# Performance work log

Hardware: AMD Instinct MI355X
Metric: run time of the kernel (lower is better)

The kernel has to match this reference:

```python
import jax, jax.numpy as jnp
import numpy as np

TOP_K = 2
INIT_STD = 0.02
B, T, D, E, I = 2, 2048, 1024, 8, 512


def setup_inputs() -> dict:
    key = jax.random.key(0)
    k0, k1, k2, k3, k4 = jax.random.split(key, 5)
    return {
        "x": jax.random.normal(k0, (B, T, D), dtype=jnp.float32),
        "router_w": (jax.random.normal(k1, (E, D), dtype=jnp.float32) * INIT_STD),
        "w_gate": (jax.random.normal(k2, (E, I, D), dtype=jnp.float32) * INIT_STD),
        "w_up": (jax.random.normal(k3, (E, I, D), dtype=jnp.float32) * INIT_STD),
        "w_down": (jax.random.normal(k4, (E, D, I), dtype=jnp.float32) * INIT_STD),
    }


def _moe_forward(x, router_w, w_gate, w_up, w_down):
    # x: [B, T, D]; router_w: [E, D]; w_gate/w_up: [E, I, D]; w_down: [E, D, I]
    b, t, d = x.shape
    e = router_w.shape[0]
    gate_logits = jnp.einsum('btd,ed->bte', x, router_w)          # [B, T, E]
    top_w, sel = jax.lax.top_k(gate_logits, TOP_K)                # [B, T, K]
    probs = jax.nn.softmax(top_w, axis=-1)                        # softmax over selected experts only

    n = b * t
    xf = x.reshape(n, d)                                          # [N, D]
    sel_f = sel.reshape(n, TOP_K)
    probs_f = probs.reshape(n, TOP_K)
    # combine weights per (token, expert); zero for unselected experts
    gates = jnp.zeros((n, e), dtype=x.dtype).at[
        jnp.arange(n)[:, None], sel_f].add(probs_f)               # [N, E]

    # SwiGLU expert FFN (no bias). Gated-dense formulation: unselected experts
    # have gate weight exactly 0, so this is bit-for-bit the same math as
    # dispatch + grouped GEMM + combine. scan over experts keeps memory at
    # one [N, I] intermediate at a time.
    def body(acc, ws):
        wg, wu, wd, g = ws                                        # [I,D],[I,D],[D,I],[N]
        h = jax.nn.silu(xf @ wg.T) * (xf @ wu.T)                  # [N, I]
        return acc + g[:, None] * (h @ wd.T), None

    out, _ = jax.lax.scan(body, jnp.zeros((n, d), dtype=x.dtype),
                          (w_gate, w_up, w_down, gates.T))
    return out.reshape(b, t, d), gate_logits


def reference(x, router_w, w_gate, w_up, w_down):
    return _moe_forward(x, router_w, w_gate, w_up, w_down)
```

## Files before the change

kernel.cpp:

```cpp
#include <hip/hip_runtime.h>
#include <cstdint>

#define N_TOK 4096
#define D_    1024
#define E_    8
#define I_    512
#define KTOP  2
#define PAD   128
#define BK    64
#define CAP   (N_TOK*KTOP + E_*PAD)
#define NBX   (CAP / PAD)
#define WSZ   ((size_t)E_ * I_ * D_)

typedef __attribute__((ext_vector_type(4))) float f32x4;
typedef __attribute__((ext_vector_type(8))) short bf16x8;

__device__ inline unsigned short f2bf(float f) {
  union { float f; uint32_t u; } v; v.f = f;
  uint32_t r = v.u + 0x7fffu + ((v.u >> 16) & 1u);
  return (unsigned short)(r >> 16);
}

#define GLOAD_LDS16(gp, lp)                                                        \
  __builtin_amdgcn_global_load_lds((const __attribute__((address_space(1))) void*)(gp), \
                                   (__attribute__((address_space(3))) void*)(lp), 16, 0, 0)

__global__ __launch_bounds__(256) void convertw_kernel(const float* __restrict__ wg,
                                                       const float* __restrict__ wu,
                                                       const float* __restrict__ wd,
                                                       unsigned short* __restrict__ dst) {
  const int y = blockIdx.y;
  const float* s = (y == 0) ? wg : (y == 1) ? wu : wd;
  unsigned short* d = dst + (size_t)y * WSZ;
  int i = blockIdx.x * 256 + threadIdx.x;
  const float4 v = reinterpret_cast<const float4*>(s)[i];
  ushort4 o;
  o.x = f2bf(v.x); o.y = f2bf(v.y); o.z = f2bf(v.z); o.w = f2bf(v.w);
  reinterpret_cast<ushort4*>(d)[i] = o;
}

__global__ __launch_bounds__(256) void router_kernel(const float* __restrict__ x,
                                                     const float* __restrict__ rw,
                                                     float* __restrict__ logits,
                                                     int* __restrict__ sel,
                                                     float* __restrict__ prob,
                                                     unsigned short* __restrict__ Xb) {
  const int lane = threadIdx.x & 63;
  const int tok  = blockIdx.x * 4 + (threadIdx.x >> 6);
  const float4* xr = reinterpret_cast<const float4*>(x + (size_t)tok * D_);
  float4 xv[4];
#pragma unroll
  for (int q = 0; q < 4; ++q) xv[q] = xr[q * 64 + lane];
  float acc[E_];
#pragma unroll
  for (int e = 0; e < E_; ++e) {
    const float4* wr = reinterpret_cast<const float4*>(rw + (size_t)e * D_);
    float s = 0.f;
#pragma unroll
    for (int q = 0; q < 4; ++q) {
      float4 wv = wr[q * 64 + lane];
      s += xv[q].x * wv.x + xv[q].y * wv.y + xv[q].z * wv.z + xv[q].w * wv.w;
    }
    acc[e] = s;
  }
  ushort4* xb = reinterpret_cast<ushort4*>(Xb + (size_t)tok * D_);
#pragma unroll
  for (int q = 0; q < 4; ++q) {
    ushort4 o;
    o.x = f2bf(xv[q].x); o.y = f2bf(xv[q].y); o.z = f2bf(xv[q].z); o.w = f2bf(xv[q].w);
    xb[q * 64 + lane] = o;
  }
#pragma unroll
  for (int e = 0; e < E_; ++e)
#pragma unroll
    for (int off = 32; off; off >>= 1) acc[e] += __shfl_xor(acc[e], off);
  if (lane == 0) {
    float v0 = -1e30f, v1 = -1e30f; int i0 = 0, i1 = 0;
#pragma unroll
    for (int e = 0; e < E_; ++e) {
      float v = acc[e];
      logits[(size_t)tok * E_ + e] = v;
      if (v > v0)      { v1 = v0; i1 = i0; v0 = v; i0 = e; }
      else if (v > v1) { v1 = v;  i1 = e; }
    }
    float t  = __expf(v1 - v0);
    sel[tok * 2] = i0; sel[tok * 2 + 1] = i1;
    prob[tok * 2] = 1.f / (1.f + t);
    prob[tok * 2 + 1] = t / (1.f + t);
  }
}

__global__ __launch_bounds__(1024) void plan_kernel(const int* __restrict__ sel,
                                                    const float* __restrict__ prob,
                                                    int* __restrict__ offs,
                                                    int* __restrict__ ptok,
                                                    float* __restrict__ pprob,
                                                    int* __restrict__ tpos,
                                                    unsigned int* __restrict__ zbuf) {
  __shared__ int wcnt[16][E_];
  __shared__ int pfx[16][E_];
  __shared__ int soffs[E_ + 1];
  __shared__ int secnt[E_];
  const int tid = threadIdx.x;
  const int wave = tid >> 6, lane = tid & 63;
  const unsigned long long lt = (1ull << lane) - 1ull;

  zbuf[tid] = 0u;

  int   mye[8];
  int   mylp[8];
  float myp[8];
  int run[E_];
#pragma unroll
  for (int e = 0; e < E_; ++e) run[e] = 0;

#pragma unroll
  for (int it = 0; it < 8; ++it) {
    int i = wave * 512 + it * 64 + lane;
    int e = sel[i];
    mye[it] = e;
    myp[it] = prob[i];
    int lp = 0;
#pragma unroll
    for (int ee = 0; ee < E_; ++ee) {
      unsigned long long m = __ballot(e == ee);
      if (e == ee) lp = run[ee] + __popcll(m & lt);
      run[ee] += __popcll(m);
    }
    mylp[it] = lp;
  }
#pragma unroll
  for (int ee = 0; ee < E_; ++ee)
    if (lane == ee) wcnt[wave][ee] = run[ee];
  __syncthreads();

  if (tid == 0) {
    int ro = 0;
#pragma unroll
    for (int e = 0; e < E_; ++e) {
      int c = 0;
      int r = ro;
      for (int w = 0; w < 16; ++w) { pfx[w][e] = r; r += wcnt[w][e]; c += wcnt[w][e]; }
      soffs[e] = ro; offs[e] = ro; secnt[e] = c;
      ro += (c + PAD - 1) & ~(PAD - 1);
    }
    soffs[E_] = ro; offs[E_] = ro;
  }
  __syncthreads();

#pragma unroll
  for (int it = 0; it < 8; ++it) {
    int i = wave * 512 + it * 64 + lane;
    int pos = pfx[wave][mye[it]] + mylp[it];
    ptok[pos]  = i >> 1;
    pprob[pos] = myp[it];
    tpos[i]    = pos;
  }
#pragma unroll
  for (int e = 0; e < E_; ++e) {
    int s = soffs[e] + secnt[e];
    int npad = soffs[e + 1] - s;
    if (tid < npad) { ptok[s + tid] = -1; pprob[s + tid] = 0.f; }
  }
}

__global__ __launch_bounds__(256) void gemm1_kernel(const unsigned short* __restrict__ Xb,
                                                    const unsigned short* __restrict__ Wg,
                                                    const unsigned short* __restrict__ Wu,
                                                    const int* __restrict__ ptok,
                                                    const int* __restrict__ offs,
                                                    const unsigned short* __restrict__ zbuf,
                                                    unsigned short* __restrict__ H) {
  __shared__ unsigned short As[PAD * BK];
  __shared__ unsigned short Bg[64 * BK];
  __shared__ unsigned short Bu[64 * BK];
  __shared__ int toks[PAD];

  const int wgid = (blockIdx.x & 7) * 72 + (blockIdx.x >> 3);
  const int bx = wgid >> 3;
  const int by = wgid & 7;

  const int total = offs[E_];
  const int t0 = bx * PAD;
  if (t0 >= total) return;
  int e = 0;
#pragma unroll
  for (int i = 1; i < E_; ++i) if (offs[i] <= t0) e = i;

  const int tid  = threadIdx.x;
  const int lane = tid & 63;
  const int w    = tid >> 6;
  if (tid < PAD) toks[tid] = ptok[t0 + tid];
  __syncthreads();

  const int ib    = by * 64;
  const int gcol8 = (lane & 7) ^ (lane >> 3);

  const unsigned short* asrc[4];
#pragma unroll
  for (int i = 0; i < 4; ++i) {
    int r = w * 32 + i * 8 + (lane >> 3);
    int t = toks[r];
    asrc[i] = (t >= 0) ? (Xb + (size_t)t * D_ + gcol8 * 8) : (zbuf + gcol8 * 8);
  }
  const unsigned short* bgsrc[2];
  const unsigned short* busrc[2];
#pragma unroll
  for (int i = 0; i < 2; ++i) {
    int r = w * 16 + i * 8 + (lane >> 3);
    size_t rowoff = ((size_t)e * I_ + ib + r) * D_ + gcol8 * 8;
    bgsrc[i] = Wg + rowoff;
    busrc[i] = Wu + rowoff;
  }

  f32x4 accg[4][2], accu[4][2];
#pragma unroll
  for (int m = 0; m < 4; ++m)
#pragma unroll
    for (int n = 0; n < 2; ++n) {
      accg[m][n] = (f32x4){0.f, 0.f, 0.f, 0.f};
      accu[m][n] = (f32x4){0.f, 0.f, 0.f, 0.f};
    }

  const int wr = w >> 1, wc = w & 1;
  const int xr7 = lane & 7;

  for (int k0 = 0; k0 < D_; k0 += BK) {
#pragma unroll
    for (int i = 0; i < 4; ++i) GLOAD_LDS16(asrc[i] + k0, &As[(w * 4 + i) * 512]);
#pragma unroll
    for (int i = 0; i < 2; ++i) {
      GLOAD_LDS16(bgsrc[i] + k0, &Bg[(w * 2 + i) * 512]);
      GLOAD_LDS16(busrc[i] + k0, &Bu[(w * 2 + i) * 512]);
    }
    __syncthreads();
#pragma unroll
    for (int kk = 0; kk < 2; ++kk) {
      const int uoff = ((kk * 4 + (lane >> 4)) ^ xr7) * 8;
      bf16x8 a[4], bg[2], bu[2];
#pragma unroll
      for (int m = 0; m < 4; ++m) {
        int row = wr * 64 + m * 16 + (lane & 15);
        a[m] = *reinterpret_cast<const bf16x8*>(&As[row * BK + uoff]);
      }
#pragma unroll
      for (int n = 0; n < 2; ++n) {
        int row = wc * 32 + n * 16 + (lane & 15);
        bg[n] = *reinterpret_cast<const bf16x8*>(&Bg[row * BK + uoff]);
        bu[n] = *reinterpret_cast<const bf16x8*>(&Bu[row * BK + uoff]);
      }
#pragma unroll
      for (int m = 0; m < 4; ++m)
#pragma unroll
        for (int n = 0; n < 2; ++n) {
          accg[m][n] = __builtin_amdgcn_mfma_f32_16x16x32_bf16(bg[n], a[m], accg[m][n], 0, 0, 0);
          accu[m][n] = __builtin_amdgcn_mfma_f32_16x16x32_bf16(bu[n], a[m], accu[m][n], 0, 0, 0);
        }
    }
    __syncthreads();
  }

#pragma unroll
  for (int m = 0; m < 4; ++m) {
    const int trow = wr * 64 + m * 16 + (lane & 15);
#pragma unroll
    for (int n = 0; n < 2; ++n) {
      const int icb = ib + wc * 32 + n * 16 + (lane >> 4) * 4;
      ushort4 st;
      float g, uu, h;
      g = accg[m][n][0]; uu = accu[m][n][0]; h = (g / (1.f + __expf(-g))) * uu; st.x = f2bf(h);
      g = accg[m][n][1]; uu = accu[m][n][1]; h = (g / (1.f + __expf(-g))) * uu; st.y = f2bf(h);
      g = accg[m][n][2]; uu = accu[m][n][2]; h = (g / (1.f + __expf(-g))) * uu; st.z = f2bf(h);
      g = accg[m][n][3]; uu = accu[m][n][3]; h = (g / (1.f + __expf(-g))) * uu; st.w = f2bf(h);
      *reinterpret_cast<ushort4*>(&H[(size_t)(t0 + trow) * I_ + icb]) = st;
    }
  }
}

__global__ __launch_bounds__(256) void gemm2_kernel(const unsigned short* __restrict__ H,
                                                    const unsigned short* __restrict__ Wd,
                                                    const float* __restrict__ pprob,
                                                    const int* __restrict__ offs,
                                                    float* __restrict__ O) {
  __shared__ unsigned short As[PAD * BK];
  __shared__ unsigned short Bs[PAD * BK];
  __shared__ float probs[PAD];

  const int wgid = (blockIdx.x & 7) * 72 + (blockIdx.x >> 3);
  const int bx = wgid >> 3;
  const int by = wgid & 7;

  const int total = offs[E_];
  const int t0 = bx * PAD;
  if (t0 >= total) return;
  int e = 0;
#pragma unroll
  for (int i = 1; i < E_; ++i) if (offs[i] <= t0) e = i;

  const int tid  = threadIdx.x;
  const int lane = tid & 63;
  const int w    = tid >> 6;
  if (tid < PAD) probs[tid] = pprob[t0 + tid];
  __syncthreads();

  const int db    = by * 128;
  const int gcol8 = (lane & 7) ^ (lane >> 3);

  const unsigned short* asrc[4];
  const unsigned short* bsrc[4];
#pragma unroll
  for (int i = 0; i < 4; ++i) {
    int r = w * 32 + i * 8 + (lane >> 3);
    asrc[i] = H + (size_t)(t0 + r) * I_ + gcol8 * 8;
    bsrc[i] = Wd + ((size_t)e * D_ + db + r) * I_ + gcol8 * 8;
  }

  f32x4 acc[4][4];
#pragma unroll
  for (int m = 0; m < 4; ++m)
#pragma unroll
    for (int n = 0; n < 4; ++n) acc[m][n] = (f32x4){0.f, 0.f, 0.f, 0.f};

  const int wr = w >> 1, wc = w & 1;
  const int xr7 = lane & 7;

  for (int k0 = 0; k0 < I_; k0 += BK) {
#pragma unroll
    for (int i = 0; i < 4; ++i) {
      GLOAD_LDS16(asrc[i] + k0, &As[(w * 4 + i) * 512]);
      GLOAD_LDS16(bsrc[i] + k0, &Bs[(w * 4 + i) * 512]);
    }
    __syncthreads();
#pragma unroll
    for (int kk = 0; kk < 2; ++kk) {
      const int uoff = ((kk * 4 + (lane >> 4)) ^ xr7) * 8;
      bf16x8 a[4], b[4];
#pragma unroll
      for (int m = 0; m < 4; ++m) {
        int row = wr * 64 + m * 16 + (lane & 15);
        a[m] = *reinterpret_cast<const bf16x8*>(&As[row * BK + uoff]);
      }
#pragma unroll
      for (int n = 0; n < 4; ++n) {
        int row = wc * 64 + n * 16 + (lane & 15);
        b[n] = *reinterpret_cast<const bf16x8*>(&Bs[row * BK + uoff]);
      }
#pragma unroll
      for (int m = 0; m < 4; ++m)
#pragma unroll
        for (int n = 0; n < 4; ++n)
          acc[m][n] = __builtin_amdgcn_mfma_f32_16x16x32_bf16(b[n], a[m], acc[m][n], 0, 0, 0);
    }
    __syncthreads();
  }

#pragma unroll
  for (int m = 0; m < 4; ++m) {
    const int trow = wr * 64 + m * 16 + (lane & 15);
    const float p = probs[trow];
#pragma unroll
    for (int n = 0; n < 4; ++n) {
      const int dcb = db + wc * 64 + n * 16 + (lane >> 4) * 4;
      float4 v;
      v.x = acc[m][n][0] * p; v.y = acc[m][n][1] * p;
      v.z = acc[m][n][2] * p; v.w = acc[m][n][3] * p;
      *reinterpret_cast<float4*>(&O[(size_t)(t0 + trow) * D_ + dcb]) = v;
    }
  }
}

__global__ __launch_bounds__(256) void combine_kernel(const float* __restrict__ O,
                                                      const int* __restrict__ tpos,
                                                      float* __restrict__ out) {
  const int t = blockIdx.x;
  const int c = threadIdx.x;
  const int p0 = tpos[2 * t], p1 = tpos[2 * t + 1];
  const float4 a = reinterpret_cast<const float4*>(O + (size_t)p0 * D_)[c];
  const float4 b = reinterpret_cast<const float4*>(O + (size_t)p1 * D_)[c];
  float4 r;
  r.x = a.x + b.x; r.y = a.y + b.y; r.z = a.z + b.z; r.w = a.w + b.w;
  reinterpret_cast<float4*>(out + (size_t)t * D_)[c] = r;
}

extern "C" void kernel_launch(void* const* d_in, const int* in_sizes, int n_in,
                              void* d_out, int out_size, void* d_ws, size_t ws_size,
                              hipStream_t stream) {
  const float* x  = (const float*)d_in[0];
  const float* rw = (const float*)d_in[1];
  const float* wg = (const float*)d_in[2];
  const float* wu = (const float*)d_in[3];
  const float* wd = (const float*)d_in[4];
  float* out    = (float*)d_out;
  float* logits = out + (size_t)N_TOK * D_;

  char* ws = (char*)d_ws;
  int*   offs  = (int*)(ws + 64);
  unsigned short* zbuf = (unsigned short*)(ws + 256);
  int*   sel   = (int*)  (ws + 4352);
  float* prob  = (float*)(ws + 37120);
  int*   ptok  = (int*)  (ws + 69888);
  float* pprob = (float*)(ws + 106752);
  int*   tpos  = (int*)  (ws + 143616);
  unsigned short* Xb  = (unsigned short*)(ws + 176384);
  unsigned short* Wgb = Xb  + (size_t)N_TOK * D_;
  unsigned short* Wub = Wgb + WSZ;
  unsigned short* Wdb = Wub + WSZ;
  unsigned short* Hb  = Wdb + WSZ;
  float* Opos = (float*)(Hb + (size_t)CAP * I_);

  convertw_kernel<<<dim3(WSZ / 4 / 256, 3), 256, 0, stream>>>(wg, wu, wd, Wgb);
  router_kernel<<<N_TOK / 4, 256, 0, stream>>>(x, rw, logits, sel, prob, Xb);
  plan_kernel<<<1, 1024, 0, stream>>>(sel, prob, offs, ptok, pprob, tpos, (unsigned int*)zbuf);
  gemm1_kernel<<<NBX * 8, 256, 0, stream>>>(Xb, Wgb, Wub, ptok, offs, zbuf, Hb);
  gemm2_kernel<<<NBX * 8, 256, 0, stream>>>(Hb, Wdb, pprob, offs, Opos);
  combine_kernel<<<N_TOK, 256, 0, stream>>>(Opos, tpos, out);
}
```

Measured before the change: 107.6 us.

## Halve expert padding tile to 64 tokens and store per-slot outputs in bf16

Reduces the per-expert padding and token tile from 128 to 64 rows, so fewer wasted padded rows are computed and the grid doubles to spread work over more CUs. Both GEMM kernels are retiled for the smaller M tile and given occupancy hints. The second GEMM now writes its per-slot outputs as bf16 instead of fp32, halving the intermediate traffic that the combine kernel reads back. The cost is lower data reuse per block, since weight tiles are reloaded twice as often, plus extra rounding error from the bf16 intermediate.

```diff
diff --git a/kernel.cpp b/kernel.cpp
--- a/kernel.cpp
+++ b/kernel.cpp
@@ -6,7 +6,7 @@
 #define E_    8
 #define I_    512
 #define KTOP  2
-#define PAD   128
+#define PAD   64
 #define BK    64
 #define CAP   (N_TOK*KTOP + E_*PAD)
 #define NBX   (CAP / PAD)
@@ -19,6 +19,10 @@
   union { float f; uint32_t u; } v; v.f = f;
   uint32_t r = v.u + 0x7fffu + ((v.u >> 16) & 1u);
   return (unsigned short)(r >> 16);
+}
+__device__ inline float bf2f(unsigned short h) {
+  union { uint32_t u; float f; } v; v.u = ((uint32_t)h) << 16;
+  return v.f;
 }
 
 #define GLOAD_LDS16(gp, lp)                                                        \
@@ -164,19 +168,19 @@
   }
 }
 
-__global__ __launch_bounds__(256) void gemm1_kernel(const unsigned short* __restrict__ Xb,
-                                                    const unsigned short* __restrict__ Wg,
-                                                    const unsigned short* __restrict__ Wu,
-                                                    const int* __restrict__ ptok,
-                                                    const int* __restrict__ offs,
-                                                    const unsigned short* __restrict__ zbuf,
-                                                    unsigned short* __restrict__ H) {
+__global__ __launch_bounds__(256, 4) void gemm1_kernel(const unsigned short* __restrict__ Xb,
+                                                       const unsigned short* __restrict__ Wg,
+                                                       const unsigned short* __restrict__ Wu,
+                                                       const int* __restrict__ ptok,
+                                                       const int* __restrict__ offs,
+                                                       const unsigned short* __restrict__ zbuf,
+                                                       unsigned short* __restrict__ H) {
   __shared__ unsigned short As[PAD * BK];
   __shared__ unsigned short Bg[64 * BK];
   __shared__ unsigned short Bu[64 * BK];
   __shared__ int toks[PAD];
 
-  const int wgid = (blockIdx.x & 7) * 72 + (blockIdx.x >> 3);
+  const int wgid = (blockIdx.x & 7) * 136 + (blockIdx.x >> 3);
   const int bx = wgid >> 3;
   const int by = wgid & 7;
 
@@ -196,26 +200,22 @@
   const int ib    = by * 64;
   const int gcol8 = (lane & 7) ^ (lane >> 3);
 
-  const unsigned short* asrc[4];
-#pragma unroll
-  for (int i = 0; i < 4; ++i) {
-    int r = w * 32 + i * 8 + (lane >> 3);
+  const unsigned short* asrc[2];
+  const unsigned short* bgsrc[2];
+  const unsigned short* busrc[2];
+#pragma unroll
+  for (int i = 0; i < 2; ++i) {
+    int r = w * 16 + i * 8 + (lane >> 3);
     int t = toks[r];
     asrc[i] = (t >= 0) ? (Xb + (size_t)t * D_ + gcol8 * 8) : (zbuf + gcol8 * 8);
-  }
-  const unsigned short* bgsrc[2];
-  const unsigned short* busrc[2];
-#pragma unroll
-  for (int i = 0; i < 2; ++i) {
-    int r = w * 16 + i * 8 + (lane >> 3);
     size_t rowoff = ((size_t)e * I_ + ib + r) * D_ + gcol8 * 8;
     bgsrc[i] = Wg + rowoff;
     busrc[i] = Wu + rowoff;
   }
 
-  f32x4 accg[4][2], accu[4][2];
-#pragma unroll
-  for (int m = 0; m < 4; ++m)
+  f32x4 accg[2][2], accu[2][2];
+#pragma unroll
+  for (int m = 0; m < 2; ++m)
 #pragma unroll
     for (int n = 0; n < 2; ++n) {
       accg[m][n] = (f32x4){0.f, 0.f, 0.f, 0.f};
@@ -227,9 +227,8 @@
 
   for (int k0 = 0; k0 < D_; k0 += BK) {
 #pragma unroll
-    for (int i = 0; i < 4; ++i) GLOAD_LDS16(asrc[i] + k0, &As[(w * 4 + i) * 512]);
-#pragma unroll
     for (int i = 0; i < 2; ++i) {
+      GLOAD_LDS16(asrc[i] + k0, &As[(w * 2 + i) * 512]);
       GLOAD_LDS16(bgsrc[i] + k0, &Bg[(w * 2 + i) * 512]);
       GLOAD_LDS16(busrc[i] + k0, &Bu[(w * 2 + i) * 512]);
     }
@@ -237,10 +236,10 @@
 #pragma unroll
     for (int kk = 0; kk < 2; ++kk) {
       const int uoff = ((kk * 4 + (lane >> 4)) ^ xr7) * 8;
-      bf16x8 a[4], bg[2], bu[2];
-#pragma unroll
-      for (int m = 0; m < 4; ++m) {
-        int row = wr * 64 + m * 16 + (lane & 15);
+      bf16x8 a[2], bg[2], bu[2];
+#pragma unroll
+      for (int m = 0; m < 2; ++m) {
+        int row = wr * 32 + m * 16 + (lane & 15);
         a[m] = *reinterpret_cast<const bf16x8*>(&As[row * BK + uoff]);
       }
 #pragma unroll
@@ -250,7 +249,7 @@
         bu[n] = *reinterpret_cast<const bf16x8*>(&Bu[row * BK + uoff]);
       }
 #pragma unroll
-      for (int m = 0; m < 4; ++m)
+      for (int m = 0; m < 2; ++m)
 #pragma unroll
         for (int n = 0; n < 2; ++n) {
           accg[m][n] = __builtin_amdgcn_mfma_f32_16x16x32_bf16(bg[n], a[m], accg[m][n], 0, 0, 0);
@@ -261,8 +260,8 @@
   }
 
 #pragma unroll
-  for (int m = 0; m < 4; ++m) {
-    const int trow = wr * 64 + m * 16 + (lane & 15);
+  for (int m = 0; m < 2; ++m) {
+    const int trow = wr * 32 + m * 16 + (lane & 15);
 #pragma unroll
     for (int n = 0; n < 2; ++n) {
       const int icb = ib + wc * 32 + n * 16 + (lane >> 4) * 4;
@@ -277,16 +276,16 @@
   }
 }
 
-__global__ __launch_bounds__(256) void gemm2_kernel(const unsigned short* __restrict__ H,
-                                                    const unsigned short* __restrict__ Wd,
-                                                    const float* __restrict__ pprob,
-                                                    const int* __restrict__ offs,
-                                                    float* __restrict__ O) {
+__global__ __launch_bounds__(256, 4) void gemm2_kernel(const unsigned short* __restrict__ H,
+                                                       const unsigned short* __restrict__ Wd,
+                                                       const float* __restrict__ pprob,
+                                                       const int* __restrict__ offs,
+                                                       unsigned short* __restrict__ O) {
   __shared__ unsigned short As[PAD * BK];
-  __shared__ unsigned short Bs[PAD * BK];
+  __shared__ unsigned short Bs[128 * BK];
   __shared__ float probs[PAD];
 
-  const int wgid = (blockIdx.x & 7) * 72 + (blockIdx.x >> 3);
+  const int wgid = (blockIdx.x & 7) * 136 + (blockIdx.x >> 3);
   const int bx = wgid >> 3;
   const int by = wgid & 7;
 
@@ -306,18 +305,22 @@
   const int db    = by * 128;
   const int gcol8 = (lane & 7) ^ (lane >> 3);
 
-  const unsigned short* asrc[4];
+  const unsigned short* asrc[2];
+#pragma unroll
+  for (int i = 0; i < 2; ++i) {
+    int r = w * 16 + i * 8 + (lane >> 3);
+    asrc[i] = H + (size_t)(t0 + r) * I_ + gcol8 * 8;
+  }
   const unsigned short* bsrc[4];
 #pragma unroll
   for (int i = 0; i < 4; ++i) {
     int r = w * 32 + i * 8 + (lane >> 3);
-    asrc[i] = H + (size_t)(t0 + r) * I_ + gcol8 * 8;
     bsrc[i] = Wd + ((size_t)e * D_ + db + r) * I_ + gcol8 * 8;
   }
 
-  f32x4 acc[4][4];
-#pragma unroll
-  for (int m = 0; m < 4; ++m)
+  f32x4 acc[2][4];
+#pragma unroll
+  for (int m = 0; m < 2; ++m)
 #pragma unroll
     for (int n = 0; n < 4; ++n) acc[m][n] = (f32x4){0.f, 0.f, 0.f, 0.f};
 
@@ -326,18 +329,17 @@
 
   for (int k0 = 0; k0 < I_; k0 += BK) {
 #pragma unroll
-    for (int i = 0; i < 4; ++i) {
-      GLOAD_LDS16(asrc[i] + k0, &As[(w * 4 + i) * 512]);
-      GLOAD_LDS16(bsrc[i] + k0, &Bs[(w * 4 + i) * 512]);
-    }
+    for (int i = 0; i < 2; ++i) GLOAD_LDS16(asrc[i] + k0, &As[(w * 2 + i) * 512]);
+#pragma unroll
+    for (int i = 0; i < 4; ++i) GLOAD_LDS16(bsrc[i] + k0, &Bs[(w * 4 + i) * 512]);
     __syncthreads();
 #pragma unroll
     for (int kk = 0; kk < 2; ++kk) {
       const int uoff = ((kk * 4 + (lane >> 4)) ^ xr7) * 8;
-      bf16x8 a[4], b[4];
-#pragma unroll
-      for (int m = 0; m < 4; ++m) {
-        int row = wr * 64 + m * 16 + (lane & 15);
+      bf16x8 a[2], b[4];
+#pragma unroll
+      for (int m = 0; m < 2; ++m) {
+        int row = wr * 32 + m * 16 + (lane & 15);
         a[m] = *reinterpret_cast<const bf16x8*>(&As[row * BK + uoff]);
       }
 #pragma unroll
@@ -346,7 +348,7 @@
         b[n] = *reinterpret_cast<const bf16x8*>(&Bs[row * BK + uoff]);
       }
 #pragma unroll
-      for (int m = 0; m < 4; ++m)
+      for (int m = 0; m < 2; ++m)
 #pragma unroll
         for (int n = 0; n < 4; ++n)
           acc[m][n] = __builtin_amdgcn_mfma_f32_16x16x32_bf16(b[n], a[m], acc[m][n], 0, 0, 0);
@@ -355,30 +357,31 @@
   }
 
 #pragma unroll
-  for (int m = 0; m < 4; ++m) {
-    const int trow = wr * 64 + m * 16 + (lane & 15);
+  for (int m = 0; m < 2; ++m) {
+    const int trow = wr * 32 + m * 16 + (lane & 15);
     const float p = probs[trow];
 #pragma unroll
     for (int n = 0; n < 4; ++n) {
       const int dcb = db + wc * 64 + n * 16 + (lane >> 4) * 4;
-      float4 v;
-      v.x = acc[m][n][0] * p; v.y = acc[m][n][1] * p;
-      v.z = acc[m][n][2] * p; v.w = acc[m][n][3] * p;
-      *reinterpret_cast<float4*>(&O[(size_t)(t0 + trow) * D_ + dcb]) = v;
-    }
-  }
-}
-
-__global__ __launch_bounds__(256) void combine_kernel(const float* __restrict__ O,
+      ushort4 v;
+      v.x = f2bf(acc[m][n][0] * p); v.y = f2bf(acc[m][n][1] * p);
+      v.z = f2bf(acc[m][n][2] * p); v.w = f2bf(acc[m][n][3] * p);
+      *reinterpret_cast<ushort4*>(&O[(size_t)(t0 + trow) * D_ + dcb]) = v;
+    }
+  }
+}
+
+__global__ __launch_bounds__(256) void combine_kernel(const unsigned short* __restrict__ O,
                                                       const int* __restrict__ tpos,
                                                       float* __restrict__ out) {
   const int t = blockIdx.x;
   const int c = threadIdx.x;
   const int p0 = tpos[2 * t], p1 = tpos[2 * t + 1];
-  const float4 a = reinterpret_cast<const float4*>(O + (size_t)p0 * D_)[c];
-  const float4 b = reinterpret_cast<const float4*>(O + (size_t)p1 * D_)[c];
+  const ushort4 a = reinterpret_cast<const ushort4*>(O + (size_t)p0 * D_)[c];
+  const ushort4 b = reinterpret_cast<const ushort4*>(O + (size_t)p1 * D_)[c];
   float4 r;
-  r.x = a.x + b.x; r.y = a.y + b.y; r.z = a.z + b.z; r.w = a.w + b.w;
+  r.x = bf2f(a.x) + bf2f(b.x); r.y = bf2f(a.y) + bf2f(b.y);
+  r.z = bf2f(a.z) + bf2f(b.z); r.w = bf2f(a.w) + bf2f(b.w);
   reinterpret_cast<float4*>(out + (size_t)t * D_)[c] = r;
 }
 
@@ -399,14 +402,14 @@
   int*   sel   = (int*)  (ws + 4352);
   float* prob  = (float*)(ws + 37120);
   int*   ptok  = (int*)  (ws + 69888);
-  float* pprob = (float*)(ws + 106752);
-  int*   tpos  = (int*)  (ws + 143616);
-  unsigned short* Xb  = (unsigned short*)(ws + 176384);
+  float* pprob = (float*)(ws + 104704);
+  int*   tpos  = (int*)  (ws + 139520);
+  unsigned short* Xb  = (unsigned short*)(ws + 172288);
   unsigned short* Wgb = Xb  + (size_t)N_TOK * D_;
   unsigned short* Wub = Wgb + WSZ;
   unsigned short* Wdb = Wub + WSZ;
   unsigned short* Hb  = Wdb + WSZ;
-  float* Opos = (float*)(Hb + (size_t)CAP * I_);
+  unsigned short* Opos = Hb + (size_t)CAP * I_;
 
   convertw_kernel<<<dim3(WSZ / 4 / 256, 3), 256, 0, stream>>>(wg, wu, wd, Wgb);
   router_kernel<<<N_TOK / 4, 256, 0, stream>>>(x, rw, logits, sel, prob, Xb);
```

After: 91.62 us. -14.8%, faster.
